# Optimization experiments

Hardware: AMD Instinct MI355X
Metric: run time of the kernel (lower is better)

The kernel has to match this reference:

```python
import jax, jax.numpy as jnp
import numpy as np

EMBED = 1024
HEADS = 16
HEAD_DIM = EMBED // HEADS
SCALE = HEAD_DIM ** -0.5


def setup_inputs() -> dict:
    key = jax.random.key(0)
    ks = jax.random.split(key, 9)
    init = lambda k, shape: jax.random.normal(k, shape, dtype=jnp.float32) * 0.02
    return {
        "hidden_states": jax.random.normal(ks[0], (32, 257, EMBED), dtype=jnp.float32),
        "Wq": init(ks[1], (EMBED, EMBED)), "bq": init(ks[2], (EMBED,)),
        "Wk": init(ks[3], (EMBED, EMBED)), "bk": init(ks[4], (EMBED,)),
        "Wv": init(ks[5], (EMBED, EMBED)), "bv": init(ks[6], (EMBED,)),
        "Wo": init(ks[7], (EMBED, EMBED)), "bo": init(ks[8], (EMBED,)),
    }


def reference(hidden_states, Wq, bq, Wk, bk, Wv, bv, Wo, bo):
    b, t, d = hidden_states.shape
    # projections (torch Linear: x @ W.T + b); scale applied to Q
    q = (hidden_states @ Wq.T + bq) * SCALE
    k = hidden_states @ Wk.T + bk
    v = hidden_states @ Wv.T + bv
    # [b, h, t, hd]
    q = q.reshape(b, t, HEADS, HEAD_DIM).transpose(0, 2, 1, 3)
    k = k.reshape(b, t, HEADS, HEAD_DIM).transpose(0, 2, 1, 3)
    v = v.reshape(b, t, HEADS, HEAD_DIM).transpose(0, 2, 1, 3)
    # attention scores + softmax (dropout p is a no-op in eval mode)
    scores = jnp.einsum("bhqd,bhkd->bhqk", q, k)
    probs = jax.nn.softmax(scores, axis=-1)
    ctx = jnp.einsum("bhqk,bhkd->bhqd", probs, v)
    ctx = ctx.transpose(0, 2, 1, 3).reshape(b, t, d)
    return ctx @ Wo.T + bo
```

## Files before the change

kernel.cpp:

```cpp
#include <hip/hip_runtime.h>


#define B_   32
#define T_   257
#define TP   272
#define H_   16
#define HD_  64
#define D_   1024
#define NTOK 8224
#define BH_  512
#define FRAG_PER_BH 17408

typedef __bf16 bf16;
typedef __bf16 bf16x4 __attribute__((ext_vector_type(4)));
typedef __bf16 bf16x8 __attribute__((ext_vector_type(8)));
typedef short  s16x4  __attribute__((ext_vector_type(4)));
typedef short  s16x8  __attribute__((ext_vector_type(8)));
typedef float  floatx4 __attribute__((ext_vector_type(4)));

static constexpr size_t SZ_XB   = (size_t)NTOK * D_ * 2;
static constexpr size_t SZ_WQKV = (size_t)3 * D_ * D_ * 2;
static constexpr size_t SZ_W    = (size_t)D_ * D_ * 2;
static constexpr size_t SZ_QK   = (size_t)BH_ * FRAG_PER_BH * 2;

static constexpr size_t OFF_XB   = 0;
static constexpr size_t OFF_WQKV = OFF_XB + SZ_XB;
static constexpr size_t OFF_WO   = OFF_WQKV + SZ_WQKV;
static constexpr size_t OFF_Q    = OFF_WO + SZ_W;
static constexpr size_t OFF_K    = OFF_Q + SZ_QK;
static constexpr size_t OFF_V    = OFF_K + SZ_QK;
static constexpr size_t OFF_CTX  = OFF_V + SZ_QK;

#define GLD16(gp, lp)                                                        \
  __builtin_amdgcn_global_load_lds(                                          \
      (const __attribute__((address_space(1))) void*)(gp),                   \
      (__attribute__((address_space(3))) void*)(lp), 16, 0, 0)

__global__ void cast_bf16_kernel(const float* __restrict__ src,
                                 bf16* __restrict__ dst, int n4) {
  int i = blockIdx.x * blockDim.x + threadIdx.x;
  int stride = gridDim.x * blockDim.x;
  for (int idx = i; idx < n4; idx += stride) {
    float4 v = reinterpret_cast<const float4*>(src)[idx];
    bf16x4 o;
    o[0] = (bf16)v.x; o[1] = (bf16)v.y; o[2] = (bf16)v.z; o[3] = (bf16)v.w;
    reinterpret_cast<bf16x4*>(dst)[idx] = o;
  }
}

__global__ void cast4_kernel(const float* __restrict__ s0, const float* __restrict__ s1,
                             const float* __restrict__ s2, const float* __restrict__ s3,
                             bf16* __restrict__ d0, bf16* __restrict__ d1,
                             bf16* __restrict__ d2, bf16* __restrict__ d3, int n4) {
  const float* s = (blockIdx.y == 0) ? s0 : (blockIdx.y == 1) ? s1
                   : (blockIdx.y == 2) ? s2 : s3;
  bf16* d = (blockIdx.y == 0) ? d0 : (blockIdx.y == 1) ? d1
            : (blockIdx.y == 2) ? d2 : d3;
  int i = blockIdx.x * blockDim.x + threadIdx.x;
  int stride = gridDim.x * blockDim.x;
  for (int idx = i; idx < n4; idx += stride) {
    float4 v = reinterpret_cast<const float4*>(s)[idx];
    bf16x4 o;
    o[0] = (bf16)v.x; o[1] = (bf16)v.y; o[2] = (bf16)v.z; o[3] = (bf16)v.w;
    reinterpret_cast<bf16x4*>(d)[idx] = o;
  }
}


__global__ __launch_bounds__(256) void qkv_gemm(
    const bf16* __restrict__ xb, const bf16* __restrict__ wqkv,
    const float* __restrict__ bq, const float* __restrict__ bk,
    const float* __restrict__ bv,
    bf16* __restrict__ Qf, bf16* __restrict__ Kf, bf16* __restrict__ Vf) {
  __shared__ bf16 smem[9216];
  bf16* Ash = smem;
  bf16* Bsh = smem + 4096;

  const int linear = blockIdx.x;
  const int nbg = ((linear & 7) * 3 + ((linear >> 3) % 3)) * 128;
  const int mbase = (linear / 24) * 128;
  const int tid = threadIdx.x;
  const int lane = tid & 63;
  const int w = tid >> 6;
  const int wr = w >> 1, wc = w & 1;
  const int n15 = lane & 15, quad = lane >> 4;

  const int lrow = lane >> 2;
  const int lseg = (lane & 3) * 8;

  floatx4 acc[4][4] = {};

  for (int k0 = 0; k0 < D_; k0 += 32) {
#pragma unroll
    for (int c = 0; c < 2; c++) {
      int r0 = w * 32 + c * 16;
      int row = r0 + lrow;
      int gm = mbase + row; if (gm > NTOK - 1) gm = NTOK - 1;
      GLD16(xb + (size_t)gm * D_ + k0 + lseg, Ash + r0 * 32);
      GLD16(wqkv + (size_t)(nbg + row) * D_ + k0 + lseg, Bsh + r0 * 32);
    }
    __syncthreads();
    bf16x8 af[4], bfr[4];
#pragma unroll
    for (int i = 0; i < 4; i++) {
      af[i]  = *reinterpret_cast<const bf16x8*>(Ash + (wr * 64 + i * 16 + n15) * 32 + quad * 8);
      bfr[i] = *reinterpret_cast<const bf16x8*>(Bsh + (wc * 64 + i * 16 + n15) * 32 + quad * 8);
    }
#pragma unroll
    for (int i = 0; i < 4; i++)
#pragma unroll
      for (int j = 0; j < 4; j++)
        acc[i][j] = __builtin_amdgcn_mfma_f32_16x16x32_bf16(af[i], bfr[j], acc[i][j], 0, 0, 0);
    __syncthreads();
  }

  const int z = nbg >> 10;
  bf16* zdst = (z == 0) ? Qf : (z == 1) ? Kf : Vf;
  const float scale = (z == 0) ? 0.125f : 1.0f;
  const float* bias = (z == 0) ? bq : (z == 1) ? bk : bv;
  const int zoff = nbg & 1023;

  const int bA = mbase / T_;
  const int tA = mbase - bA * T_;
  const int tEndA = (tA + 128 < T_) ? tA + 128 : T_;
  const int tgA0 = tA >> 4;
  const int nA = ((tEndA - 1) >> 4) - tgA0 + 1;
  int nU = nA, tEndB = 0;
  if (tA + 128 > T_ && bA + 1 < B_) {
    tEndB = tA + 128 - T_;
    nU += ((tEndB - 1) >> 4) + 1;
  }

  for (int half = 0; half < 2; half++) {
    if (wc == half) {
#pragma unroll
      for (int i = 0; i < 4; i++)
#pragma unroll
        for (int j = 0; j < 4; j++) {
          int colL = j * 16 + n15;
          float bval = bias[zoff + half * 64 + colL];
#pragma unroll
          for (int r = 0; r < 4; r++) {
            int rowL = wr * 64 + i * 16 + quad * 4 + r;
            smem[rowL * 72 + colL] = (bf16)((acc[i][j][r] + bval) * scale);
          }
        }
    }
    __syncthreads();
    const int h = (zoff >> 6) + half;
    for (int u = w; u < nU; u += 4) {
      int b, tg, tlo, thi;
      if (u < nA) {
        b = bA; tg = tgA0 + u;
        tlo = (tA > tg * 16) ? tA : tg * 16;
        int te = tg * 16 + 16; thi = (te < tEndA) ? te : tEndA;
      } else {
        b = bA + 1; tg = u - nA;
        tlo = tg * 16;
        int te = tg * 16 + 16; thi = (te < tEndB) ? te : tEndB;
      }
      bf16* gb = zdst + (size_t)(b * H_ + h) * FRAG_PER_BH + tg * 1024;
      if (z != 2) {
        int ki = lane & 15, dc = lane >> 4;
        int t = tg * 16 + ki;
        if (t >= tlo && t < thi) {
          int rowL = b * T_ + t - mbase;
          bf16x8 v0 = *reinterpret_cast<const bf16x8*>(smem + rowL * 72 + dc * 8);
          bf16x8 v1 = *reinterpret_cast<const bf16x8*>(smem + rowL * 72 + 32 + dc * 8);
          *reinterpret_cast<bf16x8*>(gb + dc * 128 + ki * 8) = v0;
          *reinterpret_cast<bf16x8*>(gb + 512 + dc * 128 + ki * 8) = v1;
        }
      } else {
        int q2 = (lane >> 4) & 3, d16 = lane & 15;
        int tb = tg * 16 + q2 * 4;
        bool full = (tb >= tlo) && (tb + 3 < thi);
#pragma unroll
        for (int p = 0; p < 2; p++) {
          bf16x8 vv;
#pragma unroll
          for (int dp = 0; dp < 2; dp++)
#pragma unroll
            for (int ki = 0; ki < 4; ki++) {
              int t = tb + ki;
              int rr = (b * T_ + t - mbase) & 127;
              vv[dp * 4 + ki] = smem[rr * 72 + p * 32 + dp * 16 + d16];
            }
          bf16* cp = gb + (p * 4 + q2) * 128 + d16 * 8;
          if (full) {
            *reinterpret_cast<bf16x8*>(cp) = vv;
          } else {
#pragma unroll
            for (int dp = 0; dp < 2; dp++)
#pragma unroll
              for (int ki = 0; ki < 4; ki++) {
                int t = tb + ki;
                if (t >= tlo && t < thi) cp[dp * 4 + ki] = vv[dp * 4 + ki];
              }
          }
        }
      }
    }
    __syncthreads();
  }
}

__global__ __launch_bounds__(256) void attn_kernel(
    const bf16* __restrict__ Qf, const bf16* __restrict__ Kf,
    const bf16* __restrict__ Vf, bf16* __restrict__ ctx) {
  __shared__ bf16 smem[34816];

  const int bh = blockIdx.x;
  const int tid = threadIdx.x;
  const int lane = tid & 63, w = tid >> 6;
  const int n15 = lane & 15, quad = lane >> 4;
  const int b = bh >> 4, h = bh & 15;

  const bf16* Qb = Qf + (size_t)bh * FRAG_PER_BH;
  const bf16* Kb = Kf + (size_t)bh * FRAG_PER_BH;
  const bf16* Vb = Vf + (size_t)bh * FRAG_PER_BH;

#pragma unroll
  for (int j = 0; j < 17; j++) {
    int c = w * 17 + j;
    const bf16* src = (c < 34) ? (Kb + c * 512) : (Vb + (c - 34) * 512);
    GLD16(src + lane * 8, smem + c * 512);
  }
  __syncthreads();
  const bf16* Ksh = smem;
  const bf16* Vsh = smem + 17408;

  const int fo = quad * 128 + n15 * 8;

  for (int qt = w; qt < 17; qt += 4) {
    bf16x8 qb0 = *reinterpret_cast<const bf16x8*>(Qb + qt * 1024 + fo);
    bf16x8 qb1 = *reinterpret_cast<const bf16x8*>(Qb + qt * 1024 + 512 + fo);

    floatx4 s[17];
#pragma unroll
    for (int kt = 0; kt < 17; kt++) {
      bf16x8 ka0 = *reinterpret_cast<const bf16x8*>(Ksh + kt * 1024 + fo);
      bf16x8 ka1 = *reinterpret_cast<const bf16x8*>(Ksh + kt * 1024 + 512 + fo);
      floatx4 c = {};
      c = __builtin_amdgcn_mfma_f32_16x16x32_bf16(ka0, qb0, c, 0, 0, 0);
      c = __builtin_amdgcn_mfma_f32_16x16x32_bf16(ka1, qb1, c, 0, 0, 0);
      s[kt] = c;
    }
    s[16][1] = -1e30f; s[16][2] = -1e30f; s[16][3] = -1e30f;
    if (quad != 0) s[16][0] = -1e30f;

    float m0 = -1e30f;
#pragma unroll
    for (int kt = 0; kt < 17; kt++)
#pragma unroll
      for (int r = 0; r < 4; r++) m0 = fmaxf(m0, s[kt][r]);
    m0 = fmaxf(m0, __shfl_xor(m0, 16));
    m0 = fmaxf(m0, __shfl_xor(m0, 32));

    float sum = 0.f;
    s16x4 pb[17];
#pragma unroll
    for (int kt = 0; kt < 17; kt++) {
      bf16x4 ph;
#pragma unroll
      for (int r = 0; r < 4; r++) {
        float p = __expf(s[kt][r] - m0);
        sum += p;
        ph[r] = (bf16)p;
      }
      pb[kt] = __builtin_bit_cast(s16x4, ph);
    }
    sum += __shfl_xor(sum, 16);
    sum += __shfl_xor(sum, 32);

    floatx4 o[4] = {};
#pragma unroll
    for (int kt = 0; kt < 17; kt++) {
#pragma unroll
      for (int p = 0; p < 2; p++) {
        bf16x8 vv = *reinterpret_cast<const bf16x8*>(
            Vsh + ((kt * 2 + p) * 4 + quad) * 128 + n15 * 8);
        s16x8 v16 = __builtin_bit_cast(s16x8, vv);
        s16x4 vlo = __builtin_shufflevector(v16, v16, 0, 1, 2, 3);
        s16x4 vhi = __builtin_shufflevector(v16, v16, 4, 5, 6, 7);
        o[p * 2]     = __builtin_amdgcn_mfma_f32_16x16x16bf16_1k(vlo, pb[kt], o[p * 2], 0, 0, 0);
        o[p * 2 + 1] = __builtin_amdgcn_mfma_f32_16x16x16bf16_1k(vhi, pb[kt], o[p * 2 + 1], 0, 0, 0);
      }
    }

    int q = qt * 16 + n15;
    if (q < T_) {
      float inv = 1.0f / sum;
      size_t ob = ((size_t)(b * T_ + q)) * D_ + h * 64 + quad * 4;
#pragma unroll
      for (int dt = 0; dt < 4; dt++) {
        bf16x4 ov;
#pragma unroll
        for (int r = 0; r < 4; r++) ov[r] = (bf16)(o[dt][r] * inv);
        *reinterpret_cast<bf16x4*>(ctx + ob + dt * 16) = ov;
      }
    }
  }
}

__global__ __launch_bounds__(256) void o_gemm(
    const bf16* __restrict__ ctx, const bf16* __restrict__ wo,
    const float* __restrict__ bo, float* __restrict__ out) {
  __shared__ bf16 Ash[128 * 32];
  __shared__ bf16 Bsh[128 * 32];

  const int linear = blockIdx.x;
  const int nbase = (linear & 7) * 128;
  const int mbase = (linear >> 3) * 128;
  const int tid = threadIdx.x;
  const int lane = tid & 63;
  const int w = tid >> 6;
  const int wr = w >> 1, wc = w & 1;
  const int n15 = lane & 15, quad = lane >> 4;

  const int lrow = lane >> 2;
  const int lseg = (lane & 3) * 8;

  floatx4 acc[4][4] = {};

  for (int k0 = 0; k0 < D_; k0 += 32) {
#pragma unroll
    for (int c = 0; c < 2; c++) {
      int r0 = w * 32 + c * 16;
      int row = r0 + lrow;
      int gm = mbase + row; if (gm > NTOK - 1) gm = NTOK - 1;
      GLD16(ctx + (size_t)gm * D_ + k0 + lseg, Ash + r0 * 32);
      GLD16(wo + (size_t)(nbase + row) * D_ + k0 + lseg, Bsh + r0 * 32);
    }
    __syncthreads();
    bf16x8 af[4], bfr[4];
#pragma unroll
    for (int i = 0; i < 4; i++) {
      af[i]  = *reinterpret_cast<const bf16x8*>(Ash + (wr * 64 + i * 16 + n15) * 32 + quad * 8);
      bfr[i] = *reinterpret_cast<const bf16x8*>(Bsh + (wc * 64 + i * 16 + n15) * 32 + quad * 8);
    }
#pragma unroll
    for (int i = 0; i < 4; i++)
#pragma unroll
      for (int j = 0; j < 4; j++)
        acc[i][j] = __builtin_amdgcn_mfma_f32_16x16x32_bf16(af[i], bfr[j], acc[i][j], 0, 0, 0);
    __syncthreads();
  }

#pragma unroll
  for (int i = 0; i < 4; i++) {
    int rowb = mbase + wr * 64 + i * 16 + quad * 4;
#pragma unroll
    for (int j = 0; j < 4; j++) {
      int col = nbase + wc * 64 + j * 16 + n15;
      float bval = bo[col];
#pragma unroll
      for (int r = 0; r < 4; r++) {
        int m = rowb + r;
        if (m < NTOK) out[(size_t)m * D_ + col] = acc[i][j][r] + bval;
      }
    }
  }
}

extern "C" void kernel_launch(void* const* d_in, const int* in_sizes, int n_in,
                              void* d_out, int out_size, void* d_ws, size_t ws_size,
                              hipStream_t stream) {
  const float* hs = (const float*)d_in[0];
  const float* Wq = (const float*)d_in[1];
  const float* bq = (const float*)d_in[2];
  const float* Wk = (const float*)d_in[3];
  const float* bk = (const float*)d_in[4];
  const float* Wv = (const float*)d_in[5];
  const float* bv = (const float*)d_in[6];
  const float* Wo = (const float*)d_in[7];
  const float* bo = (const float*)d_in[8];

  char* ws = (char*)d_ws;
  bf16* xb   = (bf16*)(ws + OFF_XB);
  bf16* wqkv = (bf16*)(ws + OFF_WQKV);
  bf16* wob  = (bf16*)(ws + OFF_WO);
  bf16* Qfw  = (bf16*)(ws + OFF_Q);
  bf16* Kfw  = (bf16*)(ws + OFF_K);
  bf16* Vfw  = (bf16*)(ws + OFF_V);
  bf16* ctx  = (bf16*)(ws + OFF_CTX);

  cast_bf16_kernel<<<2048, 256, 0, stream>>>(hs, xb, NTOK * D_ / 4);
  cast4_kernel<<<dim3(256, 4), 256, 0, stream>>>(
      Wq, Wk, Wv, Wo,
      wqkv, wqkv + (size_t)D_ * D_, wqkv + (size_t)2 * D_ * D_, wob,
      D_ * D_ / 4);

  qkv_gemm<<<1560, 256, 0, stream>>>(xb, wqkv, bq, bk, bv, Qfw, Kfw, Vfw);
  attn_kernel<<<BH_, 256, 0, stream>>>(Qfw, Kfw, Vfw, ctx);
  o_gemm<<<520, 256, 0, stream>>>(ctx, wob, bo, (float*)d_out);
}
```

Before: 252.7 us.

## Rewrite QKV GEMM as 256x256 tile with 8 waves and double-buffered ping-pong pipeline

The QKV projection GEMM moves from 128x128 tiles with 4 waves and a single-buffered 32-wide K step to 256x256 tiles with 8 waves. It uses 64-wide K tiles double-buffered in a 128KB LDS with XOR-swizzled layout, and interleaves async global-to-LDS staging with four MFMA quadrant phases using explicit barriers, waitcnt and setprio. The goal is more operand reuse per load, fewer LDS bank conflicts, and hiding memory latency behind compute. The trade-off is a grid of only 396 blocks, which risks poorer load balance and occupancy, plus fragile hand-scheduled synchronisation.

```diff
diff --git a/kernel.cpp b/kernel.cpp
--- a/kernel.cpp
+++ b/kernel.cpp
@@ -67,106 +67,198 @@
 }
 
 
-__global__ __launch_bounds__(256) void qkv_gemm(
+
+#define PH_MFMA(ACC, AF, BF)                                                 \
+  do {                                                                       \
+    __builtin_amdgcn_s_setprio(1);                                           \
+    _Pragma("unroll") for (int mi_ = 0; mi_ < 4; mi_++)                      \
+      _Pragma("unroll") for (int nj_ = 0; nj_ < 2; nj_++)                    \
+        _Pragma("unroll") for (int ks_ = 0; ks_ < 2; ks_++)                  \
+          ACC[mi_][nj_] = __builtin_amdgcn_mfma_f32_16x16x32_bf16(           \
+              AF[mi_][ks_], BF[nj_][ks_], ACC[mi_][nj_], 0, 0, 0);           \
+    __builtin_amdgcn_s_setprio(0);                                           \
+  } while (0)
+
+#define READ_A(BASE)                                                         \
+  do {                                                                       \
+    _Pragma("unroll") for (int mi_ = 0; mi_ < 4; mi_++)                      \
+      _Pragma("unroll") for (int ks_ = 0; ks_ < 2; ks_++)                    \
+        af[mi_][ks_] = *reinterpret_cast<const bf16x8*>(                     \
+            smem + (BASE) + aoffs[mi_][ks_]);                                \
+  } while (0)
+
+#define READ_B(DST, BASE)                                                    \
+  do {                                                                       \
+    _Pragma("unroll") for (int nj_ = 0; nj_ < 2; nj_++)                      \
+      _Pragma("unroll") for (int ks_ = 0; ks_ < 2; ks_++)                    \
+        DST[nj_][ks_] = *reinterpret_cast<const bf16x8*>(                    \
+            smem + (BASE) + boffs[nj_][ks_]);                                \
+  } while (0)
+
+#define LGKM0                                                                \
+  do {                                                                       \
+    asm volatile("s_waitcnt lgkmcnt(0)" ::: "memory");                       \
+    __builtin_amdgcn_sched_barrier(0);                                       \
+  } while (0)
+
+#define TILE4(TT, BB, BBN)                                                   \
+  do {                                                                       \
+    const int kt1_ = ((TT) + 1 < 16) ? (TT) + 1 : 15;                        \
+    const int kt2_ = ((TT) + 2 < 16) ? (TT) + 2 : 15;                        \
+    READ_A((BB) * 16384);                                                    \
+    READ_B(bf0, 32768 + (BB) * 16384);                                       \
+    stageA(BBN, 1, kt1_);                                                    \
+    __builtin_amdgcn_s_barrier();                                            \
+    LGKM0;                                                                   \
+    PH_MFMA(acc00, af, bf0);                                                 \
+    __builtin_amdgcn_s_barrier();                                            \
+    READ_B(bf1, 32768 + (BB) * 16384 + 8192);                                \
+    stageB(BBN, 0, kt1_);                                                    \
+    __builtin_amdgcn_s_barrier();                                            \
+    LGKM0;                                                                   \
+    PH_MFMA(acc01, af, bf1);                                                 \
+    __builtin_amdgcn_s_barrier();                                            \
+    READ_A((BB) * 16384 + 8192);                                             \
+    stageA(BB, 0, kt2_);                                                     \
+    __builtin_amdgcn_s_barrier();                                            \
+    LGKM0;                                                                   \
+    PH_MFMA(acc11, af, bf1);                                                 \
+    __builtin_amdgcn_s_barrier();                                            \
+    stageB(BB, 1, kt2_);                                                     \
+    __builtin_amdgcn_s_barrier();                                            \
+    __builtin_amdgcn_sched_barrier(0);                                       \
+    PH_MFMA(acc10, af, bf0);                                                 \
+    asm volatile("s_waitcnt vmcnt(4)" ::: "memory");                         \
+    __builtin_amdgcn_s_barrier();                                            \
+  } while (0)
+
+#define EPI_WRITE(ACC_MH0, ACC_MH1, NH)                                      \
+  do {                                                                       \
+    float bv_[2];                                                            \
+    bv_[0] = bias[znb + (NH) * 128 + wc2 * 32 + n15];                        \
+    bv_[1] = bias[znb + (NH) * 128 + wc2 * 32 + 16 + n15];                   \
+    _Pragma("unroll") for (int mi_ = 0; mi_ < 4; mi_++)                      \
+      _Pragma("unroll") for (int nj_ = 0; nj_ < 2; nj_++)                    \
+        _Pragma("unroll") for (int r_ = 0; r_ < 4; r_++) {                   \
+          int rowL_ = wr2 * 64 + mi_ * 16 + quad * 4 + r_;                   \
+          int colL_ = wc2 * 32 + nj_ * 16 + n15;                             \
+          smem[rowL_ * 136 + colL_] =                                        \
+              (bf16)((ACC_MH0[mi_][nj_][r_] + bv_[nj_]) * scale);            \
+          smem[(128 + rowL_) * 136 + colL_] =                                \
+              (bf16)((ACC_MH1[mi_][nj_][r_] + bv_[nj_]) * scale);            \
+        }                                                                    \
+  } while (0)
+
+__global__ __launch_bounds__(512, 2) void qkv_gemm(
     const bf16* __restrict__ xb, const bf16* __restrict__ wqkv,
     const float* __restrict__ bq, const float* __restrict__ bk,
     const float* __restrict__ bv,
     bf16* __restrict__ Qf, bf16* __restrict__ Kf, bf16* __restrict__ Vf) {
-  __shared__ bf16 smem[9216];
-  bf16* Ash = smem;
-  bf16* Bsh = smem + 4096;
+  __shared__ bf16 smem[65536];
 
   const int linear = blockIdx.x;
-  const int nbg = ((linear & 7) * 3 + ((linear >> 3) % 3)) * 128;
-  const int mbase = (linear / 24) * 128;
+  const int mt = linear / 12, nt = linear % 12;
+  const int m0 = mt * 256, n0 = nt * 256;
   const int tid = threadIdx.x;
-  const int lane = tid & 63;
-  const int w = tid >> 6;
-  const int wr = w >> 1, wc = w & 1;
+  const int lane = tid & 63, w = tid >> 6;
   const int n15 = lane & 15, quad = lane >> 4;
-
-  const int lrow = lane >> 2;
-  const int lseg = (lane & 3) * 8;
-
-  floatx4 acc[4][4] = {};
-
-  for (int k0 = 0; k0 < D_; k0 += 32) {
+  const int wr2 = w >> 2, wc2 = w & 3;
+  const int srow = lane >> 3, sseg = lane & 7;
+
+  auto stageA = [&](int buf, int half, int kt) {
 #pragma unroll
     for (int c = 0; c < 2; c++) {
-      int r0 = w * 32 + c * 16;
-      int row = r0 + lrow;
-      int gm = mbase + row; if (gm > NTOK - 1) gm = NTOK - 1;
-      GLD16(xb + (size_t)gm * D_ + k0 + lseg, Ash + r0 * 32);
-      GLD16(wqkv + (size_t)(nbg + row) * D_ + k0 + lseg, Bsh + r0 * 32);
-    }
-    __syncthreads();
-    bf16x8 af[4], bfr[4];
-#pragma unroll
-    for (int i = 0; i < 4; i++) {
-      af[i]  = *reinterpret_cast<const bf16x8*>(Ash + (wr * 64 + i * 16 + n15) * 32 + quad * 8);
-      bfr[i] = *reinterpret_cast<const bf16x8*>(Bsh + (wc * 64 + i * 16 + n15) * 32 + quad * 8);
-    }
-#pragma unroll
-    for (int i = 0; i < 4; i++)
-#pragma unroll
-      for (int j = 0; j < 4; j++)
-        acc[i][j] = __builtin_amdgcn_mfma_f32_16x16x32_bf16(af[i], bfr[j], acc[i][j], 0, 0, 0);
-    __syncthreads();
-  }
-
-  const int z = nbg >> 10;
+      int r = (w * 2 + c) * 8 + srow;
+      int gm = m0 + half * 128 + r; if (gm > NTOK - 1) gm = NTOK - 1;
+      int sg = (sseg ^ srow) * 8;
+      GLD16(xb + (size_t)gm * D_ + kt * 64 + sg,
+            smem + buf * 16384 + half * 8192 + (w * 2 + c) * 512);
+    }
+  };
+  auto stageB = [&](int buf, int half, int kt) {
+#pragma unroll
+    for (int c = 0; c < 2; c++) {
+      int r = (w * 2 + c) * 8 + srow;
+      int gn = n0 + half * 128 + r;
+      int sg = (sseg ^ srow) * 8;
+      GLD16(wqkv + (size_t)gn * D_ + kt * 64 + sg,
+            smem + 32768 + buf * 16384 + half * 8192 + (w * 2 + c) * 512);
+    }
+  };
+
+  int aoffs[4][2], boffs[2][2];
+#pragma unroll
+  for (int mi = 0; mi < 4; mi++)
+#pragma unroll
+    for (int ks = 0; ks < 2; ks++) {
+      int rh = wr2 * 64 + mi * 16 + n15;
+      aoffs[mi][ks] = rh * 64 + ((ks * 4 + quad) ^ (n15 & 7)) * 8;
+    }
+#pragma unroll
+  for (int nj = 0; nj < 2; nj++)
+#pragma unroll
+    for (int ks = 0; ks < 2; ks++) {
+      int rh = wc2 * 32 + nj * 16 + n15;
+      boffs[nj][ks] = rh * 64 + ((ks * 4 + quad) ^ (n15 & 7)) * 8;
+    }
+
+  floatx4 acc00[4][2] = {}, acc01[4][2] = {}, acc10[4][2] = {}, acc11[4][2] = {};
+  bf16x8 af[4][2], bf0[2][2], bf1[2][2];
+
+  stageA(0, 0, 0); stageB(0, 0, 0); stageA(0, 1, 0); stageB(0, 1, 0);
+  stageA(1, 0, 1); stageB(1, 1, 1);
+  asm volatile("s_waitcnt vmcnt(4)" ::: "memory");
+  __builtin_amdgcn_s_barrier();
+
+  for (int t = 0; t < 16; t += 2) {
+    TILE4(t, 0, 1);
+    TILE4(t + 1, 1, 0);
+  }
+
+  asm volatile("s_waitcnt vmcnt(0)" ::: "memory");
+  __builtin_amdgcn_s_barrier();
+
+  const int z = nt >> 2;
   bf16* zdst = (z == 0) ? Qf : (z == 1) ? Kf : Vf;
   const float scale = (z == 0) ? 0.125f : 1.0f;
   const float* bias = (z == 0) ? bq : (z == 1) ? bk : bv;
-  const int zoff = nbg & 1023;
-
-  const int bA = mbase / T_;
-  const int tA = mbase - bA * T_;
-  const int tEndA = (tA + 128 < T_) ? tA + 128 : T_;
+  const int znb = (nt & 3) * 256;
+
+  const int mEnd = (m0 + 256 < NTOK) ? m0 + 256 : NTOK;
+  const int span = mEnd - m0;
+  const int bA = m0 / T_;
+  const int tA = m0 - bA * T_;
+  const int tEndA = (tA + span < T_) ? tA + span : T_;
   const int tgA0 = tA >> 4;
   const int nA = ((tEndA - 1) >> 4) - tgA0 + 1;
   int nU = nA, tEndB = 0;
-  if (tA + 128 > T_ && bA + 1 < B_) {
-    tEndB = tA + 128 - T_;
+  if (tA + span > T_ && bA + 1 < B_) {
+    tEndB = tA + span - T_;
     nU += ((tEndB - 1) >> 4) + 1;
   }
 
-  for (int half = 0; half < 2; half++) {
-    if (wc == half) {
-#pragma unroll
-      for (int i = 0; i < 4; i++)
-#pragma unroll
-        for (int j = 0; j < 4; j++) {
-          int colL = j * 16 + n15;
-          float bval = bias[zoff + half * 64 + colL];
-#pragma unroll
-          for (int r = 0; r < 4; r++) {
-            int rowL = wr * 64 + i * 16 + quad * 4 + r;
-            smem[rowL * 72 + colL] = (bf16)((acc[i][j][r] + bval) * scale);
-          }
-        }
-    }
-    __syncthreads();
-    const int h = (zoff >> 6) + half;
-    for (int u = w; u < nU; u += 4) {
-      int b, tg, tlo, thi;
-      if (u < nA) {
-        b = bA; tg = tgA0 + u;
+  auto epi_store = [&](int nh_) {
+    const int h0 = (nt & 3) * 4 + nh_ * 2;
+    for (int u = w; u < nU * 2; u += 8) {
+      int g = u >> 1, hh = u & 1;
+      int bb, tg, tlo, thi;
+      if (g < nA) {
+        bb = bA; tg = tgA0 + g;
         tlo = (tA > tg * 16) ? tA : tg * 16;
         int te = tg * 16 + 16; thi = (te < tEndA) ? te : tEndA;
       } else {
-        b = bA + 1; tg = u - nA;
-        tlo = tg * 16;
+        bb = bA + 1; tg = g - nA; tlo = tg * 16;
         int te = tg * 16 + 16; thi = (te < tEndB) ? te : tEndB;
       }
-      bf16* gb = zdst + (size_t)(b * H_ + h) * FRAG_PER_BH + tg * 1024;
+      bf16* gb = zdst + (size_t)(bb * H_ + h0 + hh) * FRAG_PER_BH + tg * 1024;
+      const int hc = hh * 64;
       if (z != 2) {
         int ki = lane & 15, dc = lane >> 4;
-        int t = tg * 16 + ki;
-        if (t >= tlo && t < thi) {
-          int rowL = b * T_ + t - mbase;
-          bf16x8 v0 = *reinterpret_cast<const bf16x8*>(smem + rowL * 72 + dc * 8);
-          bf16x8 v1 = *reinterpret_cast<const bf16x8*>(smem + rowL * 72 + 32 + dc * 8);
+        int tt = tg * 16 + ki;
+        if (tt >= tlo && tt < thi) {
+          int rowL = bb * T_ + tt - m0;
+          bf16x8 v0 = *reinterpret_cast<const bf16x8*>(smem + rowL * 136 + hc + dc * 8);
+          bf16x8 v1 = *reinterpret_cast<const bf16x8*>(smem + rowL * 136 + hc + 32 + dc * 8);
           *reinterpret_cast<bf16x8*>(gb + dc * 128 + ki * 8) = v0;
           *reinterpret_cast<bf16x8*>(gb + 512 + dc * 128 + ki * 8) = v1;
         }
@@ -181,9 +273,9 @@
           for (int dp = 0; dp < 2; dp++)
 #pragma unroll
             for (int ki = 0; ki < 4; ki++) {
-              int t = tb + ki;
-              int rr = (b * T_ + t - mbase) & 127;
-              vv[dp * 4 + ki] = smem[rr * 72 + p * 32 + dp * 16 + d16];
+              int tt = tb + ki;
+              int rr = (bb * T_ + tt - m0) & 255;
+              vv[dp * 4 + ki] = smem[rr * 136 + hc + p * 32 + dp * 16 + d16];
             }
           bf16* cp = gb + (p * 4 + q2) * 128 + d16 * 8;
           if (full) {
@@ -193,15 +285,22 @@
             for (int dp = 0; dp < 2; dp++)
 #pragma unroll
               for (int ki = 0; ki < 4; ki++) {
-                int t = tb + ki;
-                if (t >= tlo && t < thi) cp[dp * 4 + ki] = vv[dp * 4 + ki];
+                int tt = tb + ki;
+                if (tt >= tlo && tt < thi) cp[dp * 4 + ki] = vv[dp * 4 + ki];
               }
           }
         }
       }
     }
-    __syncthreads();
-  }
+  };
+
+  EPI_WRITE(acc00, acc10, 0);
+  __syncthreads();
+  epi_store(0);
+  __syncthreads();
+  EPI_WRITE(acc01, acc11, 1);
+  __syncthreads();
+  epi_store(1);
 }
 
 __global__ __launch_bounds__(256) void attn_kernel(
@@ -390,7 +489,7 @@
       wqkv, wqkv + (size_t)D_ * D_, wqkv + (size_t)2 * D_ * D_, wob,
       D_ * D_ / 4);
 
-  qkv_gemm<<<1560, 256, 0, stream>>>(xb, wqkv, bq, bk, bv, Qfw, Kfw, Vfw);
+  qkv_gemm<<<396, 512, 0, stream>>>(xb, wqkv, bq, bk, bv, Qfw, Kfw, Vfw);
   attn_kernel<<<BH_, 256, 0, stream>>>(Qfw, Kfw, Vfw, ctx);
   o_gemm<<<520, 256, 0, stream>>>(ctx, wob, bo, (float*)d_out);
 }
```

Result: faster. 234.7 us (-7.1%).
